# Kernel tuning notes

Measured on AMD Instinct MI355X. Metric: run time of the kernel, lower is better.

Reference implementation:

```python
import jax, jax.numpy as jnp
import numpy as np

N = 20000       # nodes
E = 640000      # edges
H = 128         # hidden_nf = input_nf = output_nf = d_model = d_inner (expand=1)
D_STATE = 64
D_CONV = 4
DT_RANK = 8     # ceil(d_model/16) = ceil(128/16)


def setup_inputs() -> dict:
    key = jax.random.key(0)
    ks = jax.random.split(key, 20)
    g = lambda k, shape, s=0.05: jax.random.normal(k, shape, jnp.float32) * s
    return {
        'h': g(ks[0], (N, H), 1.0),
        'coord': g(ks[1], (N, 3), 1.0),
        'edge_index': jax.random.randint(ks[2], (2, E), 0, N),
        # edge_mlp: Linear(2H+1,H) ReLU Linear(H,H) ReLU
        'W_e1': g(ks[3], (H, 2 * H + 1)), 'b_e1': jnp.zeros(H, jnp.float32),
        'W_e2': g(ks[4], (H, H)), 'b_e2': jnp.zeros(H, jnp.float32),
        # att_mlp: Linear(H,1) + sigmoid
        'w_att': g(ks[5], (1, H)), 'b_att': jnp.zeros(1, jnp.float32),
        # node_mlp: Linear(2H,H) ReLU Linear(H,H)
        'W_n1': g(ks[6], (H, 2 * H)), 'b_n1': jnp.zeros(H, jnp.float32),
        'W_n2': g(ks[7], (H, H)), 'b_n2': jnp.zeros(H, jnp.float32),
        # coord_mlp: Linear(H,H) ReLU Linear(H,1,bias=False) (xavier gain 0.001)
        'W_c1': g(ks[8], (H, H)), 'b_c1': jnp.zeros(H, jnp.float32),
        'W_c2': g(ks[9], (1, H), 0.001),
        # pre_norm LayerNorm
        'ln_g': jnp.ones(H, jnp.float32), 'ln_b': jnp.zeros(H, jnp.float32),
        # Mamba(d_model=H, d_state=64, d_conv=4, expand=1)
        'in_proj_w': g(ks[10], (2 * H, H)),
        'conv_w': g(ks[11], (H, D_CONV), 0.2), 'conv_b': jnp.zeros(H, jnp.float32),
        'x_proj_w': g(ks[12], (DT_RANK + 2 * D_STATE, H)),
        'dt_proj_w': g(ks[13], (H, DT_RANK)), 'dt_proj_b': jnp.full((H,), -4.0, jnp.float32),
        'A_log': jnp.log(jnp.broadcast_to(jnp.arange(1, D_STATE + 1, dtype=jnp.float32), (H, D_STATE))),
        'D_skip': jnp.ones(H, jnp.float32),
        'out_proj_w': g(ks[14], (H, H)),
    }


def _layernorm(x, g, b):
    mu = jnp.mean(x, -1, keepdims=True)
    var = jnp.mean((x - mu) ** 2, -1, keepdims=True)
    return (x - mu) / jnp.sqrt(var + 1e-5) * g + b


def _mamba(x, in_proj_w, conv_w, conv_b, x_proj_w, dt_proj_w, dt_proj_b, A_log, D_skip, out_proj_w):
    # x: [L, H] treated as batch-1 sequence
    L = x.shape[0]
    xz = x @ in_proj_w.T                       # [L, 2H]
    u, z = xz[:, :H], xz[:, H:]
    # causal depthwise conv1d, kernel D_CONV
    up = jnp.pad(u, ((D_CONV - 1, 0), (0, 0)))
    uc = conv_b + sum(up[k:k + L] * conv_w[:, k] for k in range(D_CONV))
    uc = jax.nn.silu(uc)                       # [L, H]
    x_dbl = uc @ x_proj_w.T                    # [L, dt_rank + 2*d_state]
    dt = jax.nn.softplus(x_dbl[:, :DT_RANK] @ dt_proj_w.T + dt_proj_b)  # [L, H]
    Bm = x_dbl[:, DT_RANK:DT_RANK + D_STATE]   # [L, d_state]
    Cm = x_dbl[:, DT_RANK + D_STATE:]          # [L, d_state]
    A = -jnp.exp(A_log)                        # [H, d_state]

    def step(s, inp):
        dt_t, b_t, c_t, u_t = inp
        s = jnp.exp(dt_t[:, None] * A) * s + (dt_t * u_t)[:, None] * b_t[None, :]
        y = jnp.sum(s * c_t[None, :], -1) + D_skip * u_t
        return s, y

    _, ys = jax.lax.scan(step, jnp.zeros((H, D_STATE), jnp.float32), (dt, Bm, Cm, uc))
    y = ys * jax.nn.silu(z)
    return y @ out_proj_w.T


def reference(h, coord, edge_index, W_e1, b_e1, W_e2, b_e2, w_att, b_att,
              W_n1, b_n1, W_n2, b_n2, W_c1, b_c1, W_c2, ln_g, ln_b,
              in_proj_w, conv_w, conv_b, x_proj_w, dt_proj_w, dt_proj_b,
              A_log, D_skip, out_proj_w):
    e0, e1 = edge_index[0], edge_index[1]
    # coord2radial (norm_diff=False)
    coord_diff = coord[e0] - coord[e1]                         # [E, 3]
    radial = jnp.sum(coord_diff ** 2, 1, keepdims=True)        # [E, 1]
    # edge_model: hi = x[e0], hj = x[e1]; cat([hj, hi, radial])
    x_edge = jnp.concatenate([h[e1], h[e0], radial], axis=1)   # [E, 2H+1]
    mij = jax.nn.relu(jax.nn.relu(x_edge @ W_e1.T + b_e1) @ W_e2.T + b_e2)
    att = jax.nn.sigmoid(mij @ w_att.T + b_att)
    edge_feat = mij * att
    mi = jax.ops.segment_sum(edge_feat, e0, num_segments=N)    # [N, H]
    # coord_model (segment mean over e0)
    t = jax.nn.relu(edge_feat @ W_c1.T + b_c1) @ W_c2.T        # [E, 1]
    trans = jnp.clip(coord_diff * t, -100.0, 100.0)
    s = jax.ops.segment_sum(trans, e0, num_segments=N)
    cnt = jax.ops.segment_sum(jnp.ones_like(trans), e0, num_segments=N)
    coord_new = coord + (s / jnp.maximum(cnt, 1.0)) * 1.0      # coords_weight=1
    # node_mlp + pre_norm + clamp
    hn = jnp.concatenate([mi, h], axis=-1)
    hn = jax.nn.relu(hn @ W_n1.T + b_n1) @ W_n2.T + b_n2
    hn = _layernorm(hn, ln_g, ln_b)
    hn = jnp.clip(hn, -10.0, 10.0)
    # mamba over node sequence (bi=False, dropout=0, mamba_mlp=False)
    out = _mamba(hn, in_proj_w, conv_w, conv_b, x_proj_w, dt_proj_w,
                 dt_proj_b, A_log, D_skip, out_proj_w)
    return out, coord_new
```

## Files before the change

### kernel.cpp

```cpp
#include <hip/hip_runtime.h>
#include <math.h>

#define NN 20000
#define EE 640000
#define HD 128
#define NC 160
#define CS 125

typedef unsigned short ushort_t;
typedef __attribute__((ext_vector_type(8))) short short8v;
typedef __attribute__((ext_vector_type(4))) float f32x4;

#define MFMA16(a,b,c) __builtin_amdgcn_mfma_f32_16x16x32_bf16(a,b,c,0,0,0)

__device__ __forceinline__ float sigf(float x) { return 1.0f / (1.0f + __expf(-x)); }

__device__ __forceinline__ ushort_t f2b(float x) {
    unsigned u = __builtin_bit_cast(unsigned, x);
    unsigned r = (u + 0x7FFFu + ((u >> 16) & 1u)) >> 16;
    return (ushort_t)r;
}
__device__ __forceinline__ float b2f(ushort_t u) {
    unsigned v = ((unsigned)u) << 16;
    return __builtin_bit_cast(float, v);
}
__device__ __forceinline__ void splitf(float v, ushort_t& h, ushort_t& l) {
    h = f2b(v);
    l = f2b(v - b2f(h));
}
__device__ __forceinline__ void cvt8x2(const float* p, short8v& hi, short8v& lo) {
    #pragma unroll
    for (int j = 0; j < 8; ++j) {
        float v = p[j];
        ushort_t h, l; splitf(v, h, l);
        hi[j] = (short)h; lo[j] = (short)l;
    }
}

__global__ __launch_bounds__(1024) void prefix_kernel(const int* __restrict__ hist,
                                                      int* __restrict__ baseI)
{
    __shared__ int wsum[16];
    const int tid = threadIdx.x, lane = tid & 63, wid = tid >> 6;
    const int PER = 20;
    int i0 = tid * PER;
    int s = 0;
    for (int k = 0; k < PER; ++k) { int i = i0 + k; if (i < NN) s += hist[i]; }
    int v = s;
    #pragma unroll
    for (int off = 1; off < 64; off <<= 1) {
        int t = __shfl_up(v, off);
        if (lane >= off) v += t;
    }
    if (lane == 63) wsum[wid] = v;
    __syncthreads();
    if (tid == 0) {
        int acc = 0;
        #pragma unroll
        for (int w = 0; w < 16; ++w) { int t = wsum[w]; wsum[w] = acc; acc += t; }
    }
    __syncthreads();
    int excl = v - s + wsum[wid];
    for (int k = 0; k < PER; ++k) {
        int i = i0 + k;
        if (i < NN) { baseI[i] = excl; excl += hist[i]; }
    }
}

__global__ __launch_bounds__(256) void scatter_kernel(const int* __restrict__ ei,
                                                      const int* __restrict__ baseI,
                                                      int* __restrict__ cursor,
                                                      int* __restrict__ perm)
{
    int i = blockIdx.x * 256 + threadIdx.x;
    if (i < EE) {
        int n = ei[i];
        int p = baseI[n] + atomicAdd(&cursor[n], 1);
        perm[p] = i;
    }
}

__global__ __launch_bounds__(256) void prep_hist_kernel(
    const int* __restrict__ ei, int* __restrict__ histI,
    const float* __restrict__ We1, const float* __restrict__ We2,
    const float* __restrict__ Wc1, const float* __restrict__ Wn1,
    const float* __restrict__ Wn2, const float* __restrict__ Wip,
    const float* __restrict__ Wxp, const float* __restrict__ Wdt,
    const float* __restrict__ Wop,
    ushort_t* __restrict__ W12b, ushort_t* __restrict__ We2b,
    ushort_t* __restrict__ Wc1b,
    ushort_t* __restrict__ Wn1hi, ushort_t* __restrict__ Wn1lo,
    ushort_t* __restrict__ Wn2hi, ushort_t* __restrict__ Wn2lo,
    ushort_t* __restrict__ Wiphi, ushort_t* __restrict__ Wiplo,
    ushort_t* __restrict__ Wxp8hi, ushort_t* __restrict__ Wxp8lo,
    ushort_t* __restrict__ Wdt2hi, ushort_t* __restrict__ Wdt2lo,
    ushort_t* __restrict__ Wophi, ushort_t* __restrict__ Woplo)
{
    int i = blockIdx.x * 256 + threadIdx.x;
    if (i < EE) atomicAdd(&histI[ei[i]], 1);
    if (i < 256 * 128) {
        int j = i >> 7, k = i & 127;
        W12b[i] = f2b(We1[(j & 127) * 257 + ((j >> 7) << 7) + k]);
        ushort_t h, l;
        splitf(Wn1[i], h, l); Wn1hi[i] = h; Wn1lo[i] = l;
        splitf(Wip[i], h, l); Wiphi[i] = h; Wiplo[i] = l;
    }
    if (i < 128 * 128) {
        We2b[i] = f2b(We2[i]);
        Wc1b[i] = f2b(Wc1[i]);
        ushort_t h, l;
        splitf(Wn2[i], h, l); Wn2hi[i] = h; Wn2lo[i] = l;
        splitf(Wop[i], h, l); Wophi[i] = h; Woplo[i] = l;
        int j = i >> 7, k = i & 127;
        splitf(Wxp[(8 + j) * 128 + k], h, l); Wxp8hi[i] = h; Wxp8lo[i] = l;
        float s = 0.f;
        #pragma unroll
        for (int r = 0; r < 8; ++r) s = fmaf(Wdt[j * 8 + r], Wxp[r * 128 + k], s);
        splitf(s, h, l); Wdt2hi[i] = h; Wdt2lo[i] = l;
    }
}

__global__ __launch_bounds__(256) void p12_kernel(
    const float* __restrict__ h, const ushort_t* __restrict__ W12b,
    ushort_t* __restrict__ P12b)
{
    const int tid = threadIdx.x;
    const int lane = tid & 63;
    const int wid = tid >> 6;
    const int wm = wid >> 1, wn = wid & 1;
    const int g = lane >> 4, r16 = lane & 15;
    const int rbase = blockIdx.x * 128 + wm * 64;

    f32x4 acc[4][8];
    #pragma unroll
    for (int mt = 0; mt < 4; ++mt)
        #pragma unroll
        for (int nt = 0; nt < 8; ++nt) acc[mt][nt] = (f32x4){0.f, 0.f, 0.f, 0.f};

    for (int c = 0; c < 4; ++c) {
        short8v afr[4], bfr[8];
        #pragma unroll
        for (int mt = 0; mt < 4; ++mt) {
            int row = rbase + mt * 16 + r16;
            if (row > NN - 1) row = NN - 1;
            const float* p = h + (size_t)row * HD + c * 32 + g * 8;
            #pragma unroll
            for (int j = 0; j < 8; ++j) afr[mt][j] = (short)f2b(p[j]);
        }
        #pragma unroll
        for (int nt = 0; nt < 8; ++nt)
            bfr[nt] = *(const short8v*)(W12b + (size_t)(wn * 128 + nt * 16 + r16) * 128 + c * 32 + g * 8);
        #pragma unroll
        for (int mt = 0; mt < 4; ++mt)
            #pragma unroll
            for (int nt = 0; nt < 8; ++nt)
                acc[mt][nt] = MFMA16(afr[mt], bfr[nt], acc[mt][nt]);
    }
    #pragma unroll
    for (int mt = 0; mt < 4; ++mt)
        #pragma unroll
        for (int nt = 0; nt < 8; ++nt)
            #pragma unroll
            for (int r = 0; r < 4; ++r) {
                int row = rbase + mt * 16 + g * 4 + r;
                if (row < NN)
                    P12b[(size_t)row * 256 + wn * 128 + nt * 16 + r16] = f2b(acc[mt][nt][r]);
            }
}

__global__ __launch_bounds__(256) void edge_mfma(
    const ushort_t* __restrict__ P12b, const float* __restrict__ coord,
    const int* __restrict__ ei, const int* __restrict__ perm,
    const float* __restrict__ We1, const float* __restrict__ be1,
    const ushort_t* __restrict__ We2b, const float* __restrict__ be2,
    const float* __restrict__ watt, const float* __restrict__ batt,
    const ushort_t* __restrict__ Wc1b, const float* __restrict__ bc1,
    const float* __restrict__ Wc2,
    float* __restrict__ mi, float* __restrict__ ssum)
{
    __shared__ ushort_t ybuf[128 * 128];
    __shared__ float cdp[128][3];
    __shared__ float wcols[128], be1s[128], be2s[128], bc1s[128], watts[128], wc2s[128];
    __shared__ float pq[2][128];
    __shared__ int ej0s[128];

    const int tid = threadIdx.x;
    const int ebase = blockIdx.x * 128;
    const int lane = tid & 63;
    const int wid = tid >> 6;
    const int wm = wid >> 1, wn = wid & 1;
    const int g = lane >> 4, r16 = lane & 15;
    const float batt0 = batt[0];

    const int e = tid >> 1, hf = tid & 1;
    const int eg = perm[ebase + e];
    const int n0 = ei[eg];
    const int n1 = ei[EE + eg];
    {
        const ushort_t* p1 = P12b + (size_t)n1 * 256 + hf * 64;
        #pragma unroll
        for (int q = 0; q < 8; ++q) {
            short8v t = *(const short8v*)(p1 + q * 8);
            int off = (e << 8) + ((hf * 128 + q * 16) ^ ((e & 15) << 4));
            *(short8v*)((char*)ybuf + off) = t;
        }
    }
    if (hf == 0) ej0s[e] = n0;
    {
        int t = tid & 127;
        if (tid < 128) {
            wcols[t] = We1[t * 257 + 256];
            be1s[t] = be1[t];
            be2s[t] = be2[t];
        } else {
            bc1s[t] = bc1[t];
            watts[t] = watt[t];
            wc2s[t] = Wc2[t];
        }
    }
    float rr;
    {
        float d0 = coord[n0 * 3 + 0] - coord[n1 * 3 + 0];
        float d1 = coord[n0 * 3 + 1] - coord[n1 * 3 + 1];
        float d2 = coord[n0 * 3 + 2] - coord[n1 * 3 + 2];
        rr = d0 * d0 + d1 * d1 + d2 * d2;
        if (hf == 0) { cdp[e][0] = d0; cdp[e][1] = d1; cdp[e][2] = d2; }
    }
    __syncthreads();

    {
        short8v gb[8];
        const ushort_t* p2 = P12b + (size_t)n0 * 256 + 128 + hf * 64;
        #pragma unroll
        for (int q = 0; q < 8; ++q)
            gb[q] = *(const short8v*)(p2 + q * 8);
        const int colbase = hf * 64;
        #pragma unroll
        for (int q = 0; q < 8; ++q) {
            int off = (e << 8) + ((colbase * 2 + q * 16) ^ ((e & 15) << 4));
            short8v a = *(const short8v*)((const char*)ybuf + off);
            short8v ov;
            #pragma unroll
            for (int jj = 0; jj < 8; ++jj) {
                int col = colbase + q * 8 + jj;
                float v = b2f((ushort_t)a[jj]) + b2f((ushort_t)gb[q][jj]) + rr * wcols[col] + be1s[col];
                ov[jj] = (short)f2b(fmaxf(v, 0.f));
            }
            *(short8v*)((char*)ybuf + off) = ov;
        }
    }
    short8v b2_[4][4];
    {
        const ushort_t* W2p = We2b + (size_t)(wn * 64 + r16) * 128 + g * 8;
        #pragma unroll
        for (int nt = 0; nt < 4; ++nt)
            #pragma unroll
            for (int c = 0; c < 4; ++c)
                b2_[nt][c] = *(const short8v*)(W2p + nt * 2048 + c * 32);
    }
    __syncthreads();

    f32x4 acc[4][4];
    #pragma unroll
    for (int mt = 0; mt < 4; ++mt)
        #pragma unroll
        for (int nt = 0; nt < 4; ++nt) acc[mt][nt] = (f32x4){0.f, 0.f, 0.f, 0.f};
    #pragma unroll
    for (int c = 0; c < 4; ++c) {
        short8v afr[4];
        #pragma unroll
        for (int mt = 0; mt < 4; ++mt) {
            int row = wm * 64 + mt * 16 + r16;
            afr[mt] = *(const short8v*)((const char*)ybuf + (row << 8) + ((c * 64 + g * 16) ^ (r16 << 4)));
        }
        #pragma unroll
        for (int mt = 0; mt < 4; ++mt)
            #pragma unroll
            for (int nt = 0; nt < 4; ++nt)
                acc[mt][nt] = MFMA16(afr[mt], b2_[nt][c], acc[mt][nt]);
    }

    {
        float p[4][4];
        #pragma unroll
        for (int mt = 0; mt < 4; ++mt)
            #pragma unroll
            for (int r = 0; r < 4; ++r) p[mt][r] = 0.f;
        #pragma unroll
        for (int mt = 0; mt < 4; ++mt)
            #pragma unroll
            for (int nt = 0; nt < 4; ++nt)
                #pragma unroll
                for (int r = 0; r < 4; ++r) {
                    int col = wn * 64 + nt * 16 + r16;
                    float v = fmaxf(acc[mt][nt][r] + be2s[col], 0.f);
                    acc[mt][nt][r] = v;
                    p[mt][r] += v * watts[col];
                }
        #pragma unroll
        for (int off = 1; off < 16; off <<= 1)
            #pragma unroll
            for (int mt = 0; mt < 4; ++mt)
                #pragma unroll
                for (int r = 0; r < 4; ++r) p[mt][r] += __shfl_xor(p[mt][r], off);
        if (r16 == 0) {
            #pragma unroll
            for (int mt = 0; mt < 4; ++mt)
                #pragma unroll
                for (int r = 0; r < 4; ++r)
                    pq[wn][wm * 64 + mt * 16 + g * 4 + r] = p[mt][r];
        }
        __syncthreads();
        float att[4][4];
        #pragma unroll
        for (int mt = 0; mt < 4; ++mt)
            #pragma unroll
            for (int r = 0; r < 4; ++r) {
                int row = wm * 64 + mt * 16 + g * 4 + r;
                att[mt][r] = sigf(pq[0][row] + pq[1][row] + batt0);
            }
        __syncthreads();
        #pragma unroll
        for (int mt = 0; mt < 4; ++mt)
            #pragma unroll
            for (int nt = 0; nt < 4; ++nt)
                #pragma unroll
                for (int r = 0; r < 4; ++r) {
                    int row = wm * 64 + mt * 16 + g * 4 + r;
                    int col = wn * 64 + nt * 16 + r16;
                    int off = (row << 8) + (((col << 1)) ^ ((row & 15) << 4));
                    *(ushort_t*)((char*)ybuf + off) = f2b(acc[mt][nt][r] * att[mt][r]);
                }
    }
    __syncthreads();

    short8v b3_[4][4];
    {
        const ushort_t* W3p = Wc1b + (size_t)(wn * 64 + r16) * 128 + g * 8;
        #pragma unroll
        for (int nt = 0; nt < 4; ++nt)
            #pragma unroll
            for (int c = 0; c < 4; ++c)
                b3_[nt][c] = *(const short8v*)(W3p + nt * 2048 + c * 32);
    }

    {
        const int cp = tid & 63;
        const int qr = tid >> 6;
        const int r0 = qr * 32, r1 = r0 + 32;
        const int colbyte = cp * 4;
        float s0 = 0.f, s1 = 0.f;
        int cur = ej0s[r0];
        for (int r = r0; r < r1; ++r) {
            int node = ej0s[r];
            if (node != cur) {
                atomicAdd(&mi[(size_t)cur * HD + 2 * cp], s0);
                atomicAdd(&mi[(size_t)cur * HD + 2 * cp + 1], s1);
                s0 = 0.f; s1 = 0.f; cur = node;
            }
            int off = (r << 8) + (colbyte ^ ((r & 15) << 4));
            unsigned v = *(const unsigned*)((const char*)ybuf + off);
            s0 += b2f((ushort_t)(v & 0xFFFFu));
            s1 += b2f((ushort_t)(v >> 16));
        }
        atomicAdd(&mi[(size_t)cur * HD + 2 * cp], s0);
        atomicAdd(&mi[(size_t)cur * HD + 2 * cp + 1], s1);
    }

    #pragma unroll
    for (int mt = 0; mt < 4; ++mt)
        #pragma unroll
        for (int nt = 0; nt < 4; ++nt) acc[mt][nt] = (f32x4){0.f, 0.f, 0.f, 0.f};
    #pragma unroll
    for (int c = 0; c < 4; ++c) {
        short8v afr[4];
        #pragma unroll
        for (int mt = 0; mt < 4; ++mt) {
            int row = wm * 64 + mt * 16 + r16;
            afr[mt] = *(const short8v*)((const char*)ybuf + (row << 8) + ((c * 64 + g * 16) ^ (r16 << 4)));
        }
        #pragma unroll
        for (int mt = 0; mt < 4; ++mt)
            #pragma unroll
            for (int nt = 0; nt < 4; ++nt)
                acc[mt][nt] = MFMA16(afr[mt], b3_[nt][c], acc[mt][nt]);
    }
    {
        float q[4][4];
        #pragma unroll
        for (int mt = 0; mt < 4; ++mt)
            #pragma unroll
            for (int r = 0; r < 4; ++r) q[mt][r] = 0.f;
        #pragma unroll
        for (int mt = 0; mt < 4; ++mt)
            #pragma unroll
            for (int nt = 0; nt < 4; ++nt)
                #pragma unroll
                for (int r = 0; r < 4; ++r) {
                    int col = wn * 64 + nt * 16 + r16;
                    float v = fmaxf(acc[mt][nt][r] + bc1s[col], 0.f);
                    q[mt][r] += v * wc2s[col];
                }
        #pragma unroll
        for (int off = 1; off < 16; off <<= 1)
            #pragma unroll
            for (int mt = 0; mt < 4; ++mt)
                #pragma unroll
                for (int r = 0; r < 4; ++r) q[mt][r] += __shfl_xor(q[mt][r], off);
        if (r16 == 0) {
            #pragma unroll
            for (int mt = 0; mt < 4; ++mt)
                #pragma unroll
                for (int r = 0; r < 4; ++r)
                    pq[wn][wm * 64 + mt * 16 + g * 4 + r] = q[mt][r];
        }
        __syncthreads();
        if (tid < 48) {
            int c = tid % 3, seg = tid / 3;
            int r0 = seg * 8, r1 = r0 + 8;
            float sacc = 0.f; int cur = ej0s[r0];
            for (int r = r0; r < r1; ++r) {
                int node = ej0s[r];
                if (node != cur) {
                    atomicAdd(&ssum[cur * 3 + c], sacc);
                    sacc = 0.f; cur = node;
                }
                float tv = pq[0][r] + pq[1][r];
                float tr = cdp[r][c] * tv;
                tr = fminf(fmaxf(tr, -100.f), 100.f);
                sacc += tr;
            }
            atomicAdd(&ssum[cur * 3 + c], sacc);
        }
    }
}

__global__ __launch_bounds__(256) void node_mfma(
    const float* __restrict__ mi, const float* __restrict__ h,
    const ushort_t* __restrict__ Wn1hi, const ushort_t* __restrict__ Wn1lo,
    const float* __restrict__ bn1,
    const ushort_t* __restrict__ Wn2hi, const ushort_t* __restrict__ Wn2lo,
    const float* __restrict__ bn2,
    const float* __restrict__ lng, const float* __restrict__ lnb,
    float* __restrict__ hnf,
    const float* __restrict__ coord, const float* __restrict__ ssum,
    const int* __restrict__ histI, float* __restrict__ coordout)
{
    __shared__ ushort_t yhi[128 * 128];
    __shared__ ushort_t ylo[128 * 128];
    __shared__ float bn1s[128], bn2s[128], lngs[128], lnbs[128];

    const int tid = threadIdx.x;
    const int nbase = blockIdx.x * 128;
    const int lane = tid & 63;
    const int wid = tid >> 6;
    const int wm = wid >> 1, wn = wid & 1;
    const int g = lane >> 4, r16 = lane & 15;

    if (tid < 128) { bn1s[tid] = bn1[tid]; bn2s[tid] = bn2[tid]; lngs[tid] = lng[tid]; lnbs[tid] = lnb[tid]; }
    __syncthreads();

    f32x4 acc[4][4];
    #pragma unroll
    for (int mt = 0; mt < 4; ++mt)
        #pragma unroll
        for (int nt = 0; nt < 4; ++nt) acc[mt][nt] = (f32x4){0.f, 0.f, 0.f, 0.f};
    for (int c = 0; c < 8; ++c) {
        short8v ahi[4], alo[4], bhi[4], blo[4];
        #pragma unroll
        for (int mt = 0; mt < 4; ++mt) {
            int row = nbase + wm * 64 + mt * 16 + r16;
            if (row > NN - 1) row = NN - 1;
            const float* src = (c < 4) ? (mi + (size_t)row * HD + c * 32 + g * 8)
                                       : (h + (size_t)row * HD + (c - 4) * 32 + g * 8);
            cvt8x2(src, ahi[mt], alo[mt]);
        }
        #pragma unroll
        for (int nt = 0; nt < 4; ++nt) {
            size_t wo = (size_t)(wn * 64 + nt * 16 + r16) * 256 + c * 32 + g * 8;
            bhi[nt] = *(const short8v*)(Wn1hi + wo);
            blo[nt] = *(const short8v*)(Wn1lo + wo);
        }
        #pragma unroll
        for (int mt = 0; mt < 4; ++mt)
            #pragma unroll
            for (int nt = 0; nt < 4; ++nt) {
                acc[mt][nt] = MFMA16(ahi[mt], bhi[nt], acc[mt][nt]);
                acc[mt][nt] = MFMA16(ahi[mt], blo[nt], acc[mt][nt]);
                acc[mt][nt] = MFMA16(alo[mt], bhi[nt], acc[mt][nt]);
            }
    }
    #pragma unroll
    for (int mt = 0; mt < 4; ++mt)
        #pragma unroll
        for (int nt = 0; nt < 4; ++nt)
            #pragma unroll
            for (int r = 0; r < 4; ++r) {
                int row = wm * 64 + mt * 16 + g * 4 + r;
                int col = wn * 64 + nt * 16 + r16;
                int off = (row << 8) + (((col << 1)) ^ ((row & 15) << 4));
                float v = fmaxf(acc[mt][nt][r] + bn1s[col], 0.f);
                ushort_t hh, ll; splitf(v, hh, ll);
                *(ushort_t*)((char*)yhi + off) = hh;
                *(ushort_t*)((char*)ylo + off) = ll;
            }
    __syncthreads();

    #pragma unroll
    for (int mt = 0; mt < 4; ++mt)
        #pragma unroll
        for (int nt = 0; nt < 4; ++nt) acc[mt][nt] = (f32x4){0.f, 0.f, 0.f, 0.f};
    #pragma unroll
    for (int c = 0; c < 4; ++c) {
        short8v ahi[4], alo[4], bhi[4], blo[4];
        #pragma unroll
        for (int mt = 0; mt < 4; ++mt) {
            int row = wm * 64 + mt * 16 + r16;
            int off = (row << 8) + ((c * 64 + g * 16) ^ (r16 << 4));
            ahi[mt] = *(const short8v*)((const char*)yhi + off);
            alo[mt] = *(const short8v*)((const char*)ylo + off);
        }
        #pragma unroll
        for (int nt = 0; nt < 4; ++nt) {
            size_t wo = (size_t)(wn * 64 + nt * 16 + r16) * 128 + c * 32 + g * 8;
            bhi[nt] = *(const short8v*)(Wn2hi + wo);
            blo[nt] = *(const short8v*)(Wn2lo + wo);
        }
        #pragma unroll
        for (int mt = 0; mt < 4; ++mt)
            #pragma unroll
            for (int nt = 0; nt < 4; ++nt) {
                acc[mt][nt] = MFMA16(ahi[mt], bhi[nt], acc[mt][nt]);
                acc[mt][nt] = MFMA16(ahi[mt], blo[nt], acc[mt][nt]);
                acc[mt][nt] = MFMA16(alo[mt], bhi[nt], acc[mt][nt]);
            }
    }
    __syncthreads();
    #pragma unroll
    for (int mt = 0; mt < 4; ++mt)
        #pragma unroll
        for (int nt = 0; nt < 4; ++nt)
            #pragma unroll
            for (int r = 0; r < 4; ++r) {
                int row = wm * 64 + mt * 16 + g * 4 + r;
                int col = wn * 64 + nt * 16 + r16;
                int off = (row << 8) + (((col << 1)) ^ ((row & 15) << 4));
                float v = acc[mt][nt][r] + bn2s[col];
                ushort_t hh, ll; splitf(v, hh, ll);
                *(ushort_t*)((char*)yhi + off) = hh;
                *(ushort_t*)((char*)ylo + off) = ll;
            }
    __syncthreads();

    {
        const int row = tid >> 1, hf = tid & 1;
        const int rowg = nbase + row;
        float s1 = 0.f, s2 = 0.f;
        float vals[64];
        #pragma unroll
        for (int q = 0; q < 8; ++q) {
            int c8 = hf * 8 + q;
            int off = (row << 8) + ((c8 * 16) ^ ((row & 15) << 4));
            short8v vh = *(const short8v*)((const char*)yhi + off);
            short8v vl = *(const short8v*)((const char*)ylo + off);
            #pragma unroll
            for (int j = 0; j < 8; ++j) {
                float v = b2f((ushort_t)vh[j]) + b2f((ushort_t)vl[j]);
                vals[q * 8 + j] = v;
                s1 += v; s2 += v * v;
            }
        }
        s1 += __shfl_xor(s1, 1);
        s2 += __shfl_xor(s2, 1);
        float mu = s1 * (1.f / HD);
        float var = s2 * (1.f / HD) - mu * mu;
        float rs = rsqrtf(fmaxf(var, 0.f) + 1e-5f);
        if (rowg < NN) {
            #pragma unroll
            for (int q = 0; q < 8; ++q) {
                int c8 = hf * 8 + q;
                f32x4 o0, o1;
                #pragma unroll
                for (int j = 0; j < 8; ++j) {
                    int col = c8 * 8 + j;
                    float v = (vals[q * 8 + j] - mu) * rs * lngs[col] + lnbs[col];
                    v = fminf(fmaxf(v, -10.f), 10.f);
                    if (j < 4) o0[j] = v; else o1[j - 4] = v;
                }
                *(f32x4*)(hnf + (size_t)rowg * HD + c8 * 8) = o0;
                *(f32x4*)(hnf + (size_t)rowg * HD + c8 * 8 + 4) = o1;
            }
        }
    }

    {
        int base3 = nbase * 3;
        for (int k = tid; k < 384; k += 256) {
            int idx = base3 + k;
            if (idx < NN * 3) {
                int n = idx / 3;
                coordout[idx] = coord[idx] + ssum[idx] / fmaxf((float)histI[n], 1.f);
            }
        }
    }
}

__global__ __launch_bounds__(256) void xz_mfma(
    const float* __restrict__ hnf,
    const ushort_t* __restrict__ Wiphi, const ushort_t* __restrict__ Wiplo,
    ushort_t* __restrict__ ub, float* __restrict__ zs)
{
    const int tid = threadIdx.x;
    const int lane = tid & 63;
    const int wn = tid >> 6;
    const int g = lane >> 4, r16 = lane & 15;
    const int rbase = blockIdx.x * 64;

    f32x4 acc[4][4];
    #pragma unroll
    for (int mt = 0; mt < 4; ++mt)
        #pragma unroll
        for (int nt = 0; nt < 4; ++nt) acc[mt][nt] = (f32x4){0.f, 0.f, 0.f, 0.f};

    for (int c = 0; c < 4; ++c) {
        short8v ahi[4], alo[4], bhi[4], blo[4];
        #pragma unroll
        for (int mt = 0; mt < 4; ++mt) {
            int row = rbase + mt * 16 + r16;
            if (row > NN - 1) row = NN - 1;
            cvt8x2(hnf + (size_t)row * HD + c * 32 + g * 8, ahi[mt], alo[mt]);
        }
        #pragma unroll
        for (int nt = 0; nt < 4; ++nt) {
            size_t wo = (size_t)(wn * 64 + nt * 16 + r16) * 128 + c * 32 + g * 8;
            bhi[nt] = *(const short8v*)(Wiphi + wo);
            blo[nt] = *(const short8v*)(Wiplo + wo);
        }
        #pragma unroll
        for (int mt = 0; mt < 4; ++mt)
            #pragma unroll
            for (int nt = 0; nt < 4; ++nt) {
                acc[mt][nt] = MFMA16(ahi[mt], bhi[nt], acc[mt][nt]);
                acc[mt][nt] = MFMA16(ahi[mt], blo[nt], acc[mt][nt]);
                acc[mt][nt] = MFMA16(alo[mt], bhi[nt], acc[mt][nt]);
            }
    }
    #pragma unroll
    for (int mt = 0; mt < 4; ++mt)
        #pragma unroll
        for (int nt = 0; nt < 4; ++nt)
            #pragma unroll
            for (int r = 0; r < 4; ++r) {
                int row = rbase + mt * 16 + g * 4 + r;
                if (row >= NN) continue;
                int j = wn * 64 + nt * 16 + r16;
                float v = acc[mt][nt][r];
                if (j < HD) ub[(size_t)row * HD + j] = f2b(v);
                else        zs[(size_t)row * HD + (j - HD)] = v * sigf(v);
            }
}

__global__ __launch_bounds__(256) void convdt_mfma(
    const ushort_t* __restrict__ ub, const float* __restrict__ cw,
    const float* __restrict__ cb,
    const ushort_t* __restrict__ Wxp8hi, const ushort_t* __restrict__ Wxp8lo,
    const ushort_t* __restrict__ Wdt2hi, const ushort_t* __restrict__ Wdt2lo,
    const float* __restrict__ bdt,
    float* __restrict__ uc, float* __restrict__ Bm, float* __restrict__ Cm,
    float* __restrict__ dt)
{
    __shared__ ushort_t yhi[128 * 128];
    __shared__ ushort_t ylo[128 * 128];
    __shared__ float cws[128][4], cbs[128], bdts[128];

    const int tid = threadIdx.x;
    const int nbase = blockIdx.x * 128;
    const int lane = tid & 63;
    const int wid = tid >> 6;
    const int wm = wid >> 1, wn = wid & 1;
    const int g = lane >> 4, r16 = lane & 15;

    if (tid < 128) {
        cbs[tid] = cb[tid]; bdts[tid] = bdt[tid];
        #pragma unroll
        for (int k = 0; k < 4; ++k) cws[tid][k] = cw[tid * 4 + k];
    }
    __syncthreads();

    for (int it = tid; it < 128 * 16; it += 256) {
        int r = it >> 4, cg = it & 15;
        int t = nbase + r;
        int colb = cg * 8;
        float a[8];
        #pragma unroll
        for (int j = 0; j < 8; ++j) a[j] = cbs[colb + j];
        #pragma unroll
        for (int k = 0; k < 4; ++k) {
            int tt = t - 3 + k;
            if (tt >= 0 && tt < NN) {
                short8v uv = *(const short8v*)(ub + (size_t)tt * HD + colb);
                #pragma unroll
                for (int j = 0; j < 8; ++j) a[j] = fmaf(b2f((ushort_t)uv[j]), cws[colb + j][k], a[j]);
            }
        }
        short8v oh, ol;
        f32x4 u0, u1;
        #pragma unroll
        for (int j = 0; j < 8; ++j) {
            float s = (t < NN) ? a[j] * sigf(a[j]) : 0.f;
            ushort_t hh, ll; splitf(s, hh, ll);
            oh[j] = (short)hh; ol[j] = (short)ll;
            if (j < 4) u0[j] = s; else u1[j - 4] = s;
        }
        int off = (r << 8) + ((cg * 16) ^ ((r & 15) << 4));
        *(short8v*)((char*)yhi + off) = oh;
        *(short8v*)((char*)ylo + off) = ol;
        if (t < NN) {
            *(f32x4*)(uc + (size_t)t * HD + colb) = u0;
            *(f32x4*)(uc + (size_t)t * HD + colb + 4) = u1;
        }
    }
    __syncthreads();

    f32x4 acc[4][4];
    #pragma unroll
    for (int mt = 0; mt < 4; ++mt)
        #pragma unroll
        for (int nt = 0; nt < 4; ++nt) acc[mt][nt] = (f32x4){0.f, 0.f, 0.f, 0.f};
    #pragma unroll
    for (int c = 0; c < 4; ++c) {
        short8v ahi[4], alo[4], bhi[4], blo[4];
        #pragma unroll
        for (int mt = 0; mt < 4; ++mt) {
            int row = wm * 64 + mt * 16 + r16;
            int off = (row << 8) + ((c * 64 + g * 16) ^ (r16 << 4));
            ahi[mt] = *(const short8v*)((const char*)yhi + off);
            alo[mt] = *(const short8v*)((const char*)ylo + off);
        }
        #pragma unroll
        for (int nt = 0; nt < 4; ++nt) {
            size_t wo = (size_t)(wn * 64 + nt * 16 + r16) * 128 + c * 32 + g * 8;
            bhi[nt] = *(const short8v*)(Wxp8hi + wo);
            blo[nt] = *(const short8v*)(Wxp8lo + wo);
        }
        #pragma unroll
        for (int mt = 0; mt < 4; ++mt)
            #pragma unroll
            for (int nt = 0; nt < 4; ++nt) {
                acc[mt][nt] = MFMA16(ahi[mt], bhi[nt], acc[mt][nt]);
                acc[mt][nt] = MFMA16(ahi[mt], blo[nt], acc[mt][nt]);
                acc[mt][nt] = MFMA16(alo[mt], bhi[nt], acc[mt][nt]);
            }
    }
    #pragma unroll
    for (int mt = 0; mt < 4; ++mt)
        #pragma unroll
        for (int nt = 0; nt < 4; ++nt)
            #pragma unroll
            for (int r = 0; r < 4; ++r) {
                int row = nbase + wm * 64 + mt * 16 + g * 4 + r;
                if (row >= NN) continue;
                int j = wn * 64 + nt * 16 + r16;
                float v = acc[mt][nt][r];
                if (j < 64) Bm[(size_t)row * 64 + j] = v;
                else        Cm[(size_t)row * 64 + (j - 64)] = v;
            }

    #pragma unroll
    for (int mt = 0; mt < 4; ++mt)
        #pragma unroll
        for (int nt = 0; nt < 4; ++nt) acc[mt][nt] = (f32x4){0.f, 0.f, 0.f, 0.f};
    #pragma unroll
    for (int c = 0; c < 4; ++c) {
        short8v ahi[4], alo[4], bhi[4], blo[4];
        #pragma unroll
        for (int mt = 0; mt < 4; ++mt) {
            int row = wm * 64 + mt * 16 + r16;
            int off = (row << 8) + ((c * 64 + g * 16) ^ (r16 << 4));
            ahi[mt] = *(const short8v*)((const char*)yhi + off);
            alo[mt] = *(const short8v*)((const char*)ylo + off);
        }
        #pragma unroll
        for (int nt = 0; nt < 4; ++nt) {
            size_t wo = (size_t)(wn * 64 + nt * 16 + r16) * 128 + c * 32 + g * 8;
            bhi[nt] = *(const short8v*)(Wdt2hi + wo);
            blo[nt] = *(const short8v*)(Wdt2lo + wo);
        }
        #pragma unroll
        for (int mt = 0; mt < 4; ++mt)
            #pragma unroll
            for (int nt = 0; nt < 4; ++nt) {
                acc[mt][nt] = MFMA16(ahi[mt], bhi[nt], acc[mt][nt]);
                acc[mt][nt] = MFMA16(ahi[mt], blo[nt], acc[mt][nt]);
                acc[mt][nt] = MFMA16(alo[mt], bhi[nt], acc[mt][nt]);
            }
    }
    #pragma unroll
    for (int mt = 0; mt < 4; ++mt)
        #pragma unroll
        for (int nt = 0; nt < 4; ++nt)
            #pragma unroll
            for (int r = 0; r < 4; ++r) {
                int row = nbase + wm * 64 + mt * 16 + g * 4 + r;
                if (row >= NN) continue;
                int j = wn * 64 + nt * 16 + r16;
                float a = acc[mt][nt][r] + bdts[j];
                float sp = (a > 20.f) ? a : log1pf(__expf(a));
                dt[(size_t)row * HD + j] = sp;
            }
}

__global__ __launch_bounds__(256) void scan1_kernel(
    const float* __restrict__ dt, const float* __restrict__ uc,
    const float* __restrict__ Bm, const float* __restrict__ Alog,
    float* __restrict__ cP, float* __restrict__ cS)
{
    int g = blockIdx.x * 256 + threadIdx.x;
    int c = g >> 13;
    int r = g & 8191;
    int hh = r >> 6;
    int d = r & 63;
    float A = -__expf(Alog[hh * 64 + d]);
    float P = 1.f, S = 0.f;
    int t0 = c * CS;
    for (int t = t0; t < t0 + CS; ++t) {
        float dtv = dt[t * HD + hh];
        float a = __expf(dtv * A);
        float bv = Bm[t * 64 + d];
        float uv = uc[t * HD + hh];
        P *= a;
        S = fmaf(a, S, dtv * uv * bv);
    }
    cP[g] = P; cS[g] = S;
}

__global__ __launch_bounds__(256) void scan2_kernel(
    const float* __restrict__ cP, const float* __restrict__ cS, float* __restrict__ cI)
{
    int g = blockIdx.x * 256 + threadIdx.x;
    float S = 0.f;
    for (int c = 0; c < NC; ++c) {
        cI[c * 8192 + g] = S;
        S = fmaf(cP[c * 8192 + g], S, cS[c * 8192 + g]);
    }
}

__global__ __launch_bounds__(256) void scan3_kernel(
    const float* __restrict__ dt, const float* __restrict__ uc,
    const float* __restrict__ Bm, const float* __restrict__ Cm,
    const float* __restrict__ Alog, const float* __restrict__ Dskip,
    const float* __restrict__ cI, float* __restrict__ y)
{
    int g = blockIdx.x * 256 + threadIdx.x;
    int c = g >> 12;
    int r = g & 4095;
    int hh = r >> 5;
    int dp = (r & 31) * 2;
    float A0 = -__expf(Alog[hh * 64 + dp]);
    float A1 = -__expf(Alog[hh * 64 + dp + 1]);
    float s0 = cI[c * 8192 + hh * 64 + dp];
    float s1 = cI[c * 8192 + hh * 64 + dp + 1];
    float Dh = Dskip[hh];
    int t0 = c * CS;
    const int lane31 = threadIdx.x & 31;
    for (int t = t0; t < t0 + CS; ++t) {
        float dtv = dt[t * HD + hh];
        float uv = uc[t * HD + hh];
        float du = dtv * uv;
        float2 bv = *(const float2*)(Bm + (size_t)t * 64 + dp);
        float2 cv = *(const float2*)(Cm + (size_t)t * 64 + dp);
        s0 = fmaf(__expf(dtv * A0), s0, du * bv.x);
        s1 = fmaf(__expf(dtv * A1), s1, du * bv.y);
        float yp = fmaf(s0, cv.x, s1 * cv.y);
        #pragma unroll
        for (int off = 1; off < 32; off <<= 1) yp += __shfl_xor(yp, off);
        if (lane31 == 0) y[t * HD + hh] = yp + Dh * uv;
    }
}

__global__ __launch_bounds__(256) void out_mfma(
    const float* __restrict__ y, const float* __restrict__ zs,
    const ushort_t* __restrict__ Wophi, const ushort_t* __restrict__ Woplo,
    float* __restrict__ outp)
{
    const int tid = threadIdx.x;
    const int lane = tid & 63;
    const int wid = tid >> 6;
    const int wm = wid >> 1, wn = wid & 1;
    const int g = lane >> 4, r16 = lane & 15;
    const int nbase = blockIdx.x * 128;

    f32x4 acc[4][4];
    #pragma unroll
    for (int mt = 0; mt < 4; ++mt)
        #pragma unroll
        for (int nt = 0; nt < 4; ++nt) acc[mt][nt] = (f32x4){0.f, 0.f, 0.f, 0.f};

    for (int c = 0; c < 4; ++c) {
        short8v ahi[4], alo[4], bhi[4], blo[4];
        #pragma unroll
        for (int mt = 0; mt < 4; ++mt) {
            int row = nbase + wm * 64 + mt * 16 + r16;
            if (row > NN - 1) row = NN - 1;
            const float* yp = y + (size_t)row * HD + c * 32 + g * 8;
            const float* zp = zs + (size_t)row * HD + c * 32 + g * 8;
            #pragma unroll
            for (int j = 0; j < 8; ++j) {
                float v = yp[j] * zp[j];
                ushort_t hh, ll; splitf(v, hh, ll);
                ahi[mt][j] = (short)hh; alo[mt][j] = (short)ll;
            }
        }
        #pragma unroll
        for (int nt = 0; nt < 4; ++nt) {
            size_t wo = (size_t)(wn * 64 + nt * 16 + r16) * 128 + c * 32 + g * 8;
            bhi[nt] = *(const short8v*)(Wophi + wo);
            blo[nt] = *(const short8v*)(Woplo + wo);
        }
        #pragma unroll
        for (int mt = 0; mt < 4; ++mt)
            #pragma unroll
            for (int nt = 0; nt < 4; ++nt) {
                acc[mt][nt] = MFMA16(ahi[mt], bhi[nt], acc[mt][nt]);
                acc[mt][nt] = MFMA16(ahi[mt], blo[nt], acc[mt][nt]);
                acc[mt][nt] = MFMA16(alo[mt], bhi[nt], acc[mt][nt]);
            }
    }
    #pragma unroll
    for (int mt = 0; mt < 4; ++mt)
        #pragma unroll
        for (int nt = 0; nt < 4; ++nt)
            #pragma unroll
            for (int r = 0; r < 4; ++r) {
                int row = nbase + wm * 64 + mt * 16 + g * 4 + r;
                if (row < NN)
                    outp[(size_t)row * HD + wn * 64 + nt * 16 + r16] = acc[mt][nt][r];
            }
}

extern "C" void kernel_launch(void* const* d_in, const int* in_sizes, int n_in,
                              void* d_out, int out_size, void* d_ws, size_t ws_size,
                              hipStream_t stream)
{
    const float* h     = (const float*)d_in[0];
    const float* coord = (const float*)d_in[1];
    const int*   ei    = (const int*)d_in[2];
    const float* We1   = (const float*)d_in[3];
    const float* be1   = (const float*)d_in[4];
    const float* We2   = (const float*)d_in[5];
    const float* be2   = (const float*)d_in[6];
    const float* watt  = (const float*)d_in[7];
    const float* batt  = (const float*)d_in[8];
    const float* Wn1   = (const float*)d_in[9];
    const float* bn1   = (const float*)d_in[10];
    const float* Wn2   = (const float*)d_in[11];
    const float* bn2   = (const float*)d_in[12];
    const float* Wc1   = (const float*)d_in[13];
    const float* bc1   = (const float*)d_in[14];
    const float* Wc2   = (const float*)d_in[15];
    const float* lng   = (const float*)d_in[16];
    const float* lnb   = (const float*)d_in[17];
    const float* Wip   = (const float*)d_in[18];
    const float* convw = (const float*)d_in[19];
    const float* convb = (const float*)d_in[20];
    const float* Wxp   = (const float*)d_in[21];
    const float* Wdt   = (const float*)d_in[22];
    const float* bdt   = (const float*)d_in[23];
    const float* Alog  = (const float*)d_in[24];
    const float* Dskip = (const float*)d_in[25];
    const float* Wop   = (const float*)d_in[26];

    float* ws   = (float*)d_ws;
    float* mi   = ws;
    float* ssum = mi   + (size_t)NN * HD;
    int*   histI  = (int*)(ssum + (size_t)NN * 3);
    int*   cursor = histI + NN;
    int*   baseI  = cursor + NN;
    int*   perm   = baseI + NN;
    float* zsb  = (float*)(perm + EE);
    float* ucb  = zsb  + (size_t)NN * HD;
    float* dtb  = ucb  + (size_t)NN * HD;
    float* Bm   = dtb  + (size_t)NN * HD;
    float* Cm   = Bm   + (size_t)NN * 64;
    float* cP   = Cm   + (size_t)NN * 64;
    float* cSb  = cP   + (size_t)NC * 8192;
    float* cIb  = cSb  + (size_t)NC * 8192;
    ushort_t* ub    = (ushort_t*)(cIb + (size_t)NC * 8192);
    ushort_t* W12bp = ub + (size_t)NN * HD;
    ushort_t* We2bp = W12bp + 256 * 128;
    ushort_t* Wc1bp = We2bp + 128 * 128;
    ushort_t* Wn1hi = Wc1bp + 128 * 128;
    ushort_t* Wn1lo = Wn1hi + 128 * 256;
    ushort_t* Wn2hi = Wn1lo + 128 * 256;
    ushort_t* Wn2lo = Wn2hi + 128 * 128;
    ushort_t* Wiphi = Wn2lo + 128 * 128;
    ushort_t* Wiplo = Wiphi + 256 * 128;
    ushort_t* Wxp8hi = Wiplo + 256 * 128;
    ushort_t* Wxp8lo = Wxp8hi + 128 * 128;
    ushort_t* Wdt2hi = Wxp8lo + 128 * 128;
    ushort_t* Wdt2lo = Wdt2hi + 128 * 128;
    ushort_t* Wophi  = Wdt2lo + 128 * 128;
    ushort_t* Woplo  = Wophi + 128 * 128;
    ushort_t* P12bp = (ushort_t*)cP;
    float* hnf = cP;
    float* yb = mi;

    float* outp     = (float*)d_out;
    float* coordout = outp + (size_t)NN * HD;

    hipMemsetAsync(ws, 0, (size_t)NN * 133 * 4, stream);

    prep_hist_kernel<<<(EE + 255) / 256, 256, 0, stream>>>(ei, histI,
                                         We1, We2, Wc1, Wn1, Wn2, Wip, Wxp, Wdt, Wop,
                                         W12bp, We2bp, Wc1bp,
                                         Wn1hi, Wn1lo, Wn2hi, Wn2lo, Wiphi, Wiplo,
                                         Wxp8hi, Wxp8lo, Wdt2hi, Wdt2lo, Wophi, Woplo);
    prefix_kernel<<<1, 1024, 0, stream>>>(histI, baseI);
    scatter_kernel<<<(EE + 255) / 256, 256, 0, stream>>>(ei, baseI, cursor, perm);
    p12_kernel<<<(NN + 127) / 128, 256, 0, stream>>>(h, W12bp, P12bp);
    edge_mfma<<<EE / 128, 256, 0, stream>>>(P12bp, coord, ei, perm, We1, be1,
                                            We2bp, be2, watt, batt, Wc1bp, bc1, Wc2,
                                            mi, ssum);
    node_mfma<<<(NN + 127) / 128, 256, 0, stream>>>(mi, h, Wn1hi, Wn1lo, bn1,
                                                    Wn2hi, Wn2lo, bn2, lng, lnb, hnf,
                                                    coord, ssum, histI, coordout);
    xz_mfma<<<(NN + 63) / 64, 256, 0, stream>>>(hnf, Wiphi, Wiplo, ub, zsb);
    convdt_mfma<<<(NN + 127) / 128, 256, 0, stream>>>(ub, convw, convb,
                                                      Wxp8hi, Wxp8lo, Wdt2hi, Wdt2lo,
                                                      bdt, ucb, Bm, Cm, dtb);
    scan1_kernel<<<NC * 8192 / 256, 256, 0, stream>>>(dtb, ucb, Bm, Alog, cP, cSb);
    scan2_kernel<<<8192 / 256, 256, 0, stream>>>(cP, cSb, cIb);
    scan3_kernel<<<NC * 4096 / 256, 256, 0, stream>>>(dtb, ucb, Bm, Cm, Alog, Dskip, cIb, yb);
    out_mfma<<<(NN + 127) / 128, 256, 0, stream>>>(yb, zsb, Wophi, Woplo, outp);
}
```

Measured before the change: 647.8 us.

## Fuse Mamba in_proj GEMM into node kernel and pair states in scan1

The in_proj (xz) GEMM moves into node_mfma. The layernormed, clamped node features are kept in shared memory as a bf16 hi/lo split and fed straight to MFMA, so the fp32 hnf buffer is no longer written to and read back from global memory, and one kernel launch is dropped. Separately, scan1 now processes two state dimensions per thread with a float2 load of B, which halves the thread count and reuses the dt/u loads across both states. In exchange, node_mfma does more work per block and its occupancy may drop, and scan1 has less parallelism.

```diff
diff --git a/kernel.cpp b/kernel.cpp
--- a/kernel.cpp
+++ b/kernel.cpp
@@ -442,7 +442,8 @@
     const ushort_t* __restrict__ Wn2hi, const ushort_t* __restrict__ Wn2lo,
     const float* __restrict__ bn2,
     const float* __restrict__ lng, const float* __restrict__ lnb,
-    float* __restrict__ hnf,
+    const ushort_t* __restrict__ Wiphi, const ushort_t* __restrict__ Wiplo,
+    ushort_t* __restrict__ ub, float* __restrict__ zs,
     const float* __restrict__ coord, const float* __restrict__ ssum,
     const int* __restrict__ histI, float* __restrict__ coordout)
 {
@@ -554,7 +555,6 @@
 
     {
         const int row = tid >> 1, hf = tid & 1;
-        const int rowg = nbase + row;
         float s1 = 0.f, s2 = 0.f;
         float vals[64];
         #pragma unroll
@@ -575,21 +575,21 @@
         float mu = s1 * (1.f / HD);
         float var = s2 * (1.f / HD) - mu * mu;
         float rs = rsqrtf(fmaxf(var, 0.f) + 1e-5f);
-        if (rowg < NN) {
-            #pragma unroll
-            for (int q = 0; q < 8; ++q) {
-                int c8 = hf * 8 + q;
-                f32x4 o0, o1;
-                #pragma unroll
-                for (int j = 0; j < 8; ++j) {
-                    int col = c8 * 8 + j;
-                    float v = (vals[q * 8 + j] - mu) * rs * lngs[col] + lnbs[col];
-                    v = fminf(fmaxf(v, -10.f), 10.f);
-                    if (j < 4) o0[j] = v; else o1[j - 4] = v;
-                }
-                *(f32x4*)(hnf + (size_t)rowg * HD + c8 * 8) = o0;
-                *(f32x4*)(hnf + (size_t)rowg * HD + c8 * 8 + 4) = o1;
-            }
+        #pragma unroll
+        for (int q = 0; q < 8; ++q) {
+            int c8 = hf * 8 + q;
+            short8v oh, ol;
+            #pragma unroll
+            for (int j = 0; j < 8; ++j) {
+                int col = c8 * 8 + j;
+                float v = (vals[q * 8 + j] - mu) * rs * lngs[col] + lnbs[col];
+                v = fminf(fmaxf(v, -10.f), 10.f);
+                ushort_t hh, ll; splitf(v, hh, ll);
+                oh[j] = (short)hh; ol[j] = (short)ll;
+            }
+            int off = (row << 8) + ((c8 * 16) ^ ((row & 15) << 4));
+            *(short8v*)((char*)yhi + off) = oh;
+            *(short8v*)((char*)ylo + off) = ol;
         }
     }
 
@@ -603,61 +603,54 @@
             }
         }
     }
-}
-
-__global__ __launch_bounds__(256) void xz_mfma(
-    const float* __restrict__ hnf,
-    const ushort_t* __restrict__ Wiphi, const ushort_t* __restrict__ Wiplo,
-    ushort_t* __restrict__ ub, float* __restrict__ zs)
-{
-    const int tid = threadIdx.x;
-    const int lane = tid & 63;
-    const int wn = tid >> 6;
-    const int g = lane >> 4, r16 = lane & 15;
-    const int rbase = blockIdx.x * 64;
-
-    f32x4 acc[4][4];
-    #pragma unroll
-    for (int mt = 0; mt < 4; ++mt)
-        #pragma unroll
-        for (int nt = 0; nt < 4; ++nt) acc[mt][nt] = (f32x4){0.f, 0.f, 0.f, 0.f};
-
-    for (int c = 0; c < 4; ++c) {
-        short8v ahi[4], alo[4], bhi[4], blo[4];
-        #pragma unroll
-        for (int mt = 0; mt < 4; ++mt) {
-            int row = rbase + mt * 16 + r16;
-            if (row > NN - 1) row = NN - 1;
-            cvt8x2(hnf + (size_t)row * HD + c * 32 + g * 8, ahi[mt], alo[mt]);
-        }
-        #pragma unroll
-        for (int nt = 0; nt < 4; ++nt) {
-            size_t wo = (size_t)(wn * 64 + nt * 16 + r16) * 128 + c * 32 + g * 8;
-            bhi[nt] = *(const short8v*)(Wiphi + wo);
-            blo[nt] = *(const short8v*)(Wiplo + wo);
-        }
-        #pragma unroll
-        for (int mt = 0; mt < 4; ++mt)
+    __syncthreads();
+
+    #pragma unroll
+    for (int jh = 0; jh < 2; ++jh) {
+        #pragma unroll
+        for (int mt = 0; mt < 4; ++mt)
+            #pragma unroll
+            for (int nt = 0; nt < 4; ++nt) acc[mt][nt] = (f32x4){0.f, 0.f, 0.f, 0.f};
+        #pragma unroll
+        for (int c = 0; c < 4; ++c) {
+            short8v ahi[4], alo[4], bhi[4], blo[4];
+            #pragma unroll
+            for (int mt = 0; mt < 4; ++mt) {
+                int row = wm * 64 + mt * 16 + r16;
+                int off = (row << 8) + ((c * 64 + g * 16) ^ (r16 << 4));
+                ahi[mt] = *(const short8v*)((const char*)yhi + off);
+                alo[mt] = *(const short8v*)((const char*)ylo + off);
+            }
             #pragma unroll
             for (int nt = 0; nt < 4; ++nt) {
-                acc[mt][nt] = MFMA16(ahi[mt], bhi[nt], acc[mt][nt]);
-                acc[mt][nt] = MFMA16(ahi[mt], blo[nt], acc[mt][nt]);
-                acc[mt][nt] = MFMA16(alo[mt], bhi[nt], acc[mt][nt]);
-            }
-    }
-    #pragma unroll
-    for (int mt = 0; mt < 4; ++mt)
-        #pragma unroll
-        for (int nt = 0; nt < 4; ++nt)
-            #pragma unroll
-            for (int r = 0; r < 4; ++r) {
-                int row = rbase + mt * 16 + g * 4 + r;
-                if (row >= NN) continue;
-                int j = wn * 64 + nt * 16 + r16;
-                float v = acc[mt][nt][r];
-                if (j < HD) ub[(size_t)row * HD + j] = f2b(v);
-                else        zs[(size_t)row * HD + (j - HD)] = v * sigf(v);
-            }
+                int j = wn * 128 + jh * 64 + nt * 16 + r16;
+                size_t wo = (size_t)j * 128 + c * 32 + g * 8;
+                bhi[nt] = *(const short8v*)(Wiphi + wo);
+                blo[nt] = *(const short8v*)(Wiplo + wo);
+            }
+            #pragma unroll
+            for (int mt = 0; mt < 4; ++mt)
+                #pragma unroll
+                for (int nt = 0; nt < 4; ++nt) {
+                    acc[mt][nt] = MFMA16(ahi[mt], bhi[nt], acc[mt][nt]);
+                    acc[mt][nt] = MFMA16(ahi[mt], blo[nt], acc[mt][nt]);
+                    acc[mt][nt] = MFMA16(alo[mt], bhi[nt], acc[mt][nt]);
+                }
+        }
+        #pragma unroll
+        for (int mt = 0; mt < 4; ++mt)
+            #pragma unroll
+            for (int nt = 0; nt < 4; ++nt)
+                #pragma unroll
+                for (int r = 0; r < 4; ++r) {
+                    int row = nbase + wm * 64 + mt * 16 + g * 4 + r;
+                    if (row >= NN) continue;
+                    int j = wn * 128 + jh * 64 + nt * 16 + r16;
+                    float v = acc[mt][nt][r];
+                    if (j < HD) ub[(size_t)row * HD + j] = f2b(v);
+                    else        zs[(size_t)row * HD + (j - HD)] = v * sigf(v);
+                }
+    }
 }
 
 __global__ __launch_bounds__(256) void convdt_mfma(
@@ -816,22 +809,27 @@
     float* __restrict__ cP, float* __restrict__ cS)
 {
     int g = blockIdx.x * 256 + threadIdx.x;
-    int c = g >> 13;
-    int r = g & 8191;
-    int hh = r >> 6;
-    int d = r & 63;
-    float A = -__expf(Alog[hh * 64 + d]);
-    float P = 1.f, S = 0.f;
+    int c = g >> 12;
+    int r = g & 4095;
+    int hh = r >> 5;
+    int dp = (r & 31) * 2;
+    float A0 = -__expf(Alog[hh * 64 + dp]);
+    float A1 = -__expf(Alog[hh * 64 + dp + 1]);
+    float P0 = 1.f, S0 = 0.f, P1 = 1.f, S1 = 0.f;
     int t0 = c * CS;
     for (int t = t0; t < t0 + CS; ++t) {
         float dtv = dt[t * HD + hh];
-        float a = __expf(dtv * A);
-        float bv = Bm[t * 64 + d];
         float uv = uc[t * HD + hh];
-        P *= a;
-        S = fmaf(a, S, dtv * uv * bv);
-    }
-    cP[g] = P; cS[g] = S;
+        float du = dtv * uv;
+        float2 bv = *(const float2*)(Bm + (size_t)t * 64 + dp);
+        float a0 = __expf(dtv * A0);
+        float a1 = __expf(dtv * A1);
+        P0 *= a0; P1 *= a1;
+        S0 = fmaf(a0, S0, du * bv.x);
+        S1 = fmaf(a1, S1, du * bv.y);
+    }
+    *(float2*)(cP + (size_t)c * 8192 + hh * 64 + dp) = make_float2(P0, P1);
+    *(float2*)(cS + (size_t)c * 8192 + hh * 64 + dp) = make_float2(S0, S1);
 }
 
 __global__ __launch_bounds__(256) void scan2_kernel(
@@ -1002,7 +1000,6 @@
     ushort_t* Wophi  = Wdt2lo + 128 * 128;
     ushort_t* Woplo  = Wophi + 128 * 128;
     ushort_t* P12bp = (ushort_t*)cP;
-    float* hnf = cP;
     float* yb = mi;
 
     float* outp     = (float*)d_out;
@@ -1022,13 +1019,13 @@
                                             We2bp, be2, watt, batt, Wc1bp, bc1, Wc2,
                                             mi, ssum);
     node_mfma<<<(NN + 127) / 128, 256, 0, stream>>>(mi, h, Wn1hi, Wn1lo, bn1,
-                                                    Wn2hi, Wn2lo, bn2, lng, lnb, hnf,
+                                                    Wn2hi, Wn2lo, bn2, lng, lnb,
+                                                    Wiphi, Wiplo, ub, zsb,
                                                     coord, ssum, histI, coordout);
-    xz_mfma<<<(NN + 63) / 64, 256, 0, stream>>>(hnf, Wiphi, Wiplo, ub, zsb);
     convdt_mfma<<<(NN + 127) / 128, 256, 0, stream>>>(ub, convw, convb,
                                                       Wxp8hi, Wxp8lo, Wdt2hi, Wdt2lo,
                                                       bdt, ucb, Bm, Cm, dtb);
-    scan1_kernel<<<NC * 8192 / 256, 256, 0, stream>>>(dtb, ucb, Bm, Alog, cP, cSb);
+    scan1_kernel<<<NC * 4096 / 256, 256, 0, stream>>>(dtb, ucb, Bm, Alog, cP, cSb);
     scan2_kernel<<<8192 / 256, 256, 0, stream>>>(cP, cSb, cIb);
     scan3_kernel<<<NC * 4096 / 256, 256, 0, stream>>>(dtb, ucb, Bm, Cm, Alog, Dskip, cIb, yb);
     out_mfma<<<(NN + 127) / 128, 256, 0, stream>>>(yb, zsb, Wophi, Woplo, outp);
```

After: 639.5 us. Within noise of the previous version (-1.3%).
